# Optimization experiments

Hardware: AMD Instinct MI355X
Metric: run time of the kernel (lower is better)

## Reference

```python
import jax, jax.numpy as jnp
import numpy as np

N = 100000      # nodes
E = 1600000     # edges
F_IN = 128      # num_features
H = 64          # hidden_channels
EPS = 1e-5      # batchnorm eps


def _bn(x, gamma, beta, mean, var):
    # inference-mode BatchNorm1d
    return (x - mean) * jax.lax.rsqrt(var + EPS) * gamma + beta


def setup_inputs() -> dict:
    key = jax.random.key(0)
    ks = jax.random.split(key, 16)

    def lin_w(k, fan_in, fan_out):
        return (jax.random.normal(k, (fan_in, fan_out), jnp.float32)
                * (1.0 / np.sqrt(fan_in)))

    return {
        "x": jax.random.normal(ks[0], (N, F_IN), jnp.float32),
        "edge_index": jax.random.randint(ks[1], (2, E), 0, N, dtype=jnp.int32),
        # node_encoder: Linear(F_IN,H) + BN
        "enc_W": lin_w(ks[2], F_IN, H), "enc_b": jnp.zeros((H,), jnp.float32),
        "enc_g": jnp.ones((H,), jnp.float32), "enc_beta": jnp.zeros((H,), jnp.float32),
        "enc_mean": jnp.zeros((H,), jnp.float32), "enc_var": jnp.ones((H,), jnp.float32),
        # GCNConv layers (PyG: lin without bias, bias added after aggregation)
        "conv1_W": lin_w(ks[3], H, H), "conv1_b": jnp.zeros((H,), jnp.float32),
        "conv2_W": lin_w(ks[4], H, H), "conv2_b": jnp.zeros((H,), jnp.float32),
        # edge_predictor: Linear(2H,H) + BN + Linear(H,1)
        "ep1_W": lin_w(ks[5], 2 * H, H), "ep1_b": jnp.zeros((H,), jnp.float32),
        "ep_g": jnp.ones((H,), jnp.float32), "ep_beta": jnp.zeros((H,), jnp.float32),
        "ep_mean": jnp.zeros((H,), jnp.float32), "ep_var": jnp.ones((H,), jnp.float32),
        "ep2_W": lin_w(ks[6], H, 1), "ep2_b": jnp.zeros((1,), jnp.float32),
    }


def reference(x, edge_index, enc_W, enc_b, enc_g, enc_beta, enc_mean, enc_var,
              conv1_W, conv1_b, conv2_W, conv2_b,
              ep1_W, ep1_b, ep_g, ep_beta, ep_mean, ep_var, ep2_W, ep2_b):
    row, col = edge_index[0], edge_index[1]

    # GCN normalization with added self-loops (symmetric D^-1/2 (A+I) D^-1/2)
    loops = jnp.arange(N, dtype=row.dtype)
    row_sl = jnp.concatenate([row, loops])          # [E+N]
    col_sl = jnp.concatenate([col, loops])
    deg = jax.ops.segment_sum(jnp.ones_like(col_sl, jnp.float32), col_sl, N)
    dinv = jnp.where(deg > 0, jax.lax.rsqrt(jnp.maximum(deg, 1.0)), 0.0)
    norm = dinv[row_sl] * dinv[col_sl]              # [E+N]

    def gcn_conv(h, W, b):
        hw = h @ W                                   # [N,H]
        msg = hw[row_sl] * norm[:, None]             # gather-scale  [E+N,H]
        return jax.ops.segment_sum(msg, col_sl, N) + b  # scatter-add

    # node encoder (inference: dropout = identity)
    h = jax.nn.relu(_bn(x @ enc_W + enc_b, enc_g, enc_beta, enc_mean, enc_var))
    h = jax.nn.relu(gcn_conv(h, conv1_W, conv1_b))
    h = jax.nn.relu(gcn_conv(h, conv2_W, conv2_b))
    node_embeddings = h

    # edge predictor: gather + cat + MLP + sigmoid
    ef = jnp.concatenate([h[row], h[col]], axis=1)   # [E, 2H]
    e = jax.nn.relu(_bn(ef @ ep1_W + ep1_b, ep_g, ep_beta, ep_mean, ep_var))
    edge_pred = jax.nn.sigmoid(e @ ep2_W + ep2_b)    # [E, 1]
    return node_embeddings, edge_pred
```

## Files before the change

### kernel.cpp

```cpp
#include <hip/hip_runtime.h>
#include <hip/hip_bf16.h>
#include <hip/hip_fp16.h>

#define NN 100000
#define NE 1600000
#define FIN 128
#define HD 64
#define NB_MF 1563
#define BSH 8
#define BUCK 256
#define NBUCK 392
#define BCAP 5120
#define CHUNK 4096
#define NCHUNK 391
#define ESPLIT 2
#define NEB (NBUCK*ESPLIT)
#define NFB 6250
#define NAGG 6250

typedef unsigned int uint32;
typedef _Float16 half8 __attribute__((ext_vector_type(8)));
typedef float f32x4 __attribute__((ext_vector_type(4)));
typedef float f32x8 __attribute__((ext_vector_type(8)));

__global__ void __launch_bounds__(256) k_prep(const float* __restrict__ encW, const float* __restrict__ c1W,
                                              const float* __restrict__ c2W, const float* __restrict__ ep1W,
                                              _Float16* __restrict__ wt,
                                              const float* __restrict__ encB, const float* __restrict__ encG,
                                              const float* __restrict__ encBe, const float* __restrict__ encM,
                                              const float* __restrict__ encV,
                                              const float* __restrict__ ep1b, const float* __restrict__ epG,
                                              const float* __restrict__ epBe, const float* __restrict__ epM,
                                              const float* __restrict__ epV,
                                              float* __restrict__ foldEnc, float* __restrict__ foldPre,
                                              int* __restrict__ bcnt, _Float16* __restrict__ bufBzero){
    int blk = blockIdx.x, t = threadIdx.x;
    if(blk < 96){
        int i = blk*256 + t;
        if(i < 8192){
            int n = i >> 7, k = i & 127;
            wt[i] = (_Float16)encW[k*64 + n];
        } else if(i < 12288){
            int j = i - 8192; int n = j >> 6, k = j & 63;
            wt[i] = (_Float16)c1W[k*64 + n];
        } else if(i < 16384){
            int j = i - 12288; int n = j >> 6, k = j & 63;
            wt[i] = (_Float16)c2W[k*64 + n];
        } else {
            int j = i - 16384; int h = j >> 12; int jj = j & 4095;
            int n = jj >> 6, k = jj & 63;
            wt[i] = (_Float16)ep1W[(h*64 + k)*64 + n];
        }
    } else {
        if(t < 64){
            int j = t;
            float s = encG[j]*rsqrtf(encV[j]+1e-5f);
            foldEnc[j]      = s;
            foldEnc[64+j]   = (encB[j]-encM[j])*s + encBe[j];
            float sp = epG[j]*rsqrtf(epV[j]+1e-5f);
            foldPre[j]      = sp;
            foldPre[64+j]   = sp;
            foldPre[128+j]  = sp*(ep1b[j]-epM[j]) + epBe[j];
            foldPre[192+j]  = 0.f;
            bufBzero[j]     = (_Float16)0.f;
        }
        for(int i = t; i < NBUCK; i += 256) bcnt[i] = 0;
    }
}

__global__ void __launch_bounds__(256) k_part(const int* __restrict__ row,
                                              const int* __restrict__ col,
                                              int* __restrict__ bcnt,
                                              uint32* __restrict__ staged,
                                              uint32* __restrict__ posE){
    __shared__ int hist[NBUCK];
    __shared__ int base[NBUCK];
    int t = threadIdx.x;
    int e0 = blockIdx.x * CHUNK;
    int e1 = min(e0 + CHUNK, NE);
    for(int i = t; i < NBUCK; i += 256) hist[i] = 0;
    __syncthreads();
    for(int e = e0 + t; e < e1; e += 256)
        atomicAdd(&hist[col[e] >> BSH], 1);
    __syncthreads();
    for(int i = t; i < NBUCK; i += 256){
        int c = hist[i];
        base[i] = (c > 0) ? atomicAdd(&bcnt[i], c) : 0;
        hist[i] = 0;
    }
    __syncthreads();
    for(int e = e0 + t; e < e1; e += 256){
        int c = col[e], r = row[e];
        int b = c >> BSH;
        int pos = base[b] + atomicAdd(&hist[b], 1);
        if(pos < BCAP){
            staged[(size_t)b*BCAP + pos] = ((uint32)r << BSH) | (uint32)(c & (BUCK-1));
            posE[e] = (uint32)(b*BCAP + pos);
        } else posE[e] = 0xFFFFFFFFu;
    }
}

__global__ void __launch_bounds__(256) k_fill3(const int* __restrict__ bcnt,
                                               const uint32* __restrict__ staged,
                                               int* __restrict__ deg,
                                               int* __restrict__ starts,
                                               float* __restrict__ dinv,
                                               int* __restrict__ csr){
    __shared__ int h[BUCK];
    __shared__ int sc[BUCK];
    __shared__ int red[256];
    __shared__ int lcsr[BCAP];
    int b = blockIdx.x, t = threadIdx.x;
    int part = 0;
    for(int i = t; i < b; i += 256) part += min(bcnt[i], BCAP);
    red[t] = part; __syncthreads();
    for(int off = 128; off > 0; off >>= 1){
        if(t < off) red[t] += red[t+off];
        __syncthreads();
    }
    int base = red[0];
    h[t] = 0;
    __syncthreads();
    int cnt = min(bcnt[b], BCAP);
    const uint32* st = staged + (size_t)b*BCAP;
    for(int i = t; i < cnt; i += 256) atomicAdd(&h[st[i] & (BUCK-1)], 1);
    __syncthreads();
    int v = h[t];
    sc[t] = v; __syncthreads();
    for(int off = 1; off < 256; off <<= 1){
        int a = (t >= off) ? sc[t-off] : 0;
        __syncthreads();
        sc[t] += a;
        __syncthreads();
    }
    int ex = sc[t] - v;
    int n = b*BUCK + t;
    if(n < NN){
        deg[n]    = v;
        starts[n] = base + ex;
        dinv[n]   = rsqrtf((float)(v + 1));
    }
    h[t] = ex;
    __syncthreads();
    for(int i = t; i < cnt; i += 256){
        uint32 u = st[i];
        int p = atomicAdd(&h[u & (BUCK-1)], 1);
        lcsr[p] = (int)(u >> BSH);
    }
    __syncthreads();
    for(int i = t; i < cnt; i += 256) csr[base + i] = lcsr[i];
}

template<int K, bool AF32, bool FOLD, bool RELU, bool SCALE, int OS>
__global__ void __launch_bounds__(256) k_mfma(const void* __restrict__ Ain,
                                              const _Float16* __restrict__ Bt,
                                              const float* __restrict__ fold,
                                              const float* __restrict__ rowscale,
                                              _Float16* __restrict__ outh){
    constexpr int PS = K + 8;
    __shared__ _Float16 As[64*PS];
    __shared__ _Float16 Bs[64*PS];
    int t = threadIdx.x;
    int m0 = blockIdx.x*64;
    int jh = blockIdx.y;
    {
        const _Float16* src = Bt + (size_t)jh*64*K;
        for(int idx = t; idx < 64*(K/8); idx += 256){
            int n = idx/(K/8), c = idx%(K/8);
            *(half8*)&Bs[n*PS + c*8] = *(const half8*)&src[n*K + c*8];
        }
    }
    if(AF32){
        const float* A = (const float*)Ain;
        for(int idx = t; idx < 64*(K/4); idx += 256){
            int r = idx/(K/4), c = idx%(K/4);
            int rowi = m0 + r; if(rowi >= NN) rowi = NN-1;
            float4 v = *(const float4*)&A[(size_t)rowi*K + c*4];
            _Float16* d = &As[r*PS + c*4];
            d[0]=(_Float16)v.x; d[1]=(_Float16)v.y; d[2]=(_Float16)v.z; d[3]=(_Float16)v.w;
        }
    } else {
        const _Float16* A = (const _Float16*)Ain;
        for(int idx = t; idx < 64*(K/8); idx += 256){
            int r = idx/(K/8), c = idx%(K/8);
            int rowi = m0 + r; if(rowi >= NN) rowi = NN-1;
            *(half8*)&As[r*PS + c*8] = *(const half8*)&A[(size_t)rowi*K + c*8];
        }
    }
    __syncthreads();
    int w = t>>6, l = t&63;
    int lm = l&15, q = l>>4;
    f32x4 acc0 = {0.f,0.f,0.f,0.f}, acc1 = {0.f,0.f,0.f,0.f};
    f32x4 acc2 = {0.f,0.f,0.f,0.f}, acc3 = {0.f,0.f,0.f,0.f};
    const _Float16* arow = &As[(w*16+lm)*PS + q*8];
    const _Float16* brow = &Bs[lm*PS + q*8];
    #pragma unroll
    for(int ks = 0; ks < K/32; ks++){
        half8 a  = *(const half8*)(arow + ks*32);
        half8 b0 = *(const half8*)(brow + ks*32);
        half8 b1 = *(const half8*)(brow + 16*PS + ks*32);
        half8 b2 = *(const half8*)(brow + 32*PS + ks*32);
        half8 b3 = *(const half8*)(brow + 48*PS + ks*32);
        acc0 = __builtin_amdgcn_mfma_f32_16x16x32_f16(a, b0, acc0, 0,0,0);
        acc1 = __builtin_amdgcn_mfma_f32_16x16x32_f16(a, b1, acc1, 0,0,0);
        acc2 = __builtin_amdgcn_mfma_f32_16x16x32_f16(a, b2, acc2, 0,0,0);
        acc3 = __builtin_amdgcn_mfma_f32_16x16x32_f16(a, b3, acc3, 0,0,0);
    }
    f32x4 accs[4] = {acc0, acc1, acc2, acc3};
    #pragma unroll
    for(int nt = 0; nt < 4; nt++){
        int col = nt*16 + lm;
        int jcol = jh*64 + col;
        float fs = FOLD ? fold[jcol] : 0.f;
        float fb = FOLD ? fold[OS + jcol] : 0.f;
        #pragma unroll
        for(int r = 0; r < 4; r++){
            int rowi = m0 + w*16 + q*4 + r;
            if(rowi >= NN) continue;
            float v = accs[nt][r];
            if(FOLD) v = v*fs + fb;
            if(RELU) v = fmaxf(v, 0.f);
            if(SCALE) v *= rowscale[rowi];
            outh[(size_t)rowi*OS + jcol] = (_Float16)v;
        }
    }
}

__global__ void __launch_bounds__(256) k_agg4(const _Float16* __restrict__ hb,
                                              const int* __restrict__ starts,
                                              const int* __restrict__ deg,
                                              const int* __restrict__ csr,
                                              const float* __restrict__ dinv,
                                              const float* __restrict__ bias,
                                              _Float16* __restrict__ outh,
                                              float* __restrict__ outf){
    int t = threadIdx.x, w = t>>6, f = t&63;
    int n0 = blockIdx.x*16 + w*4;
    int s0 = __builtin_amdgcn_readfirstlane(starts[n0+0]);
    int s1 = __builtin_amdgcn_readfirstlane(starts[n0+1]);
    int s2 = __builtin_amdgcn_readfirstlane(starts[n0+2]);
    int s3 = __builtin_amdgcn_readfirstlane(starts[n0+3]);
    int d0 = __builtin_amdgcn_readfirstlane(deg[n0+0]);
    int d1 = __builtin_amdgcn_readfirstlane(deg[n0+1]);
    int d2 = __builtin_amdgcn_readfirstlane(deg[n0+2]);
    int d3 = __builtin_amdgcn_readfirstlane(deg[n0+3]);
    float a0 = 0.f, a1 = 0.f, a2 = 0.f, a3 = 0.f;
    int dmax = max(max(d0,d1), max(d2,d3));
    for(int i0 = 0; i0 < dmax; i0 += 64){
        int li0 = (i0+f < d0) ? csr[s0+i0+f] : NN;
        int li1 = (i0+f < d1) ? csr[s1+i0+f] : NN;
        int li2 = (i0+f < d2) ? csr[s2+i0+f] : NN;
        int li3 = (i0+f < d3) ? csr[s3+i0+f] : NN;
        int mm = min(dmax - i0, 64);
        for(int j = 0; j < mm; j += 8){
            float t0 = 0.f, t1 = 0.f, t2 = 0.f, t3 = 0.f;
            #pragma unroll
            for(int u = 0; u < 8; u++){
                int r0 = __builtin_amdgcn_readlane(li0, j+u);
                int r1 = __builtin_amdgcn_readlane(li1, j+u);
                int r2 = __builtin_amdgcn_readlane(li2, j+u);
                int r3 = __builtin_amdgcn_readlane(li3, j+u);
                t0 += (float)hb[(size_t)r0*64 + f];
                t1 += (float)hb[(size_t)r1*64 + f];
                t2 += (float)hb[(size_t)r2*64 + f];
                t3 += (float)hb[(size_t)r3*64 + f];
            }
            a0 += t0; a1 += t1; a2 += t2; a3 += t3;
        }
    }
    float bv = bias[f];
    float dn0 = dinv[n0+0], dn1 = dinv[n0+1], dn2 = dinv[n0+2], dn3 = dinv[n0+3];
    float sf0 = (float)hb[(size_t)(n0+0)*64 + f];
    float sf1 = (float)hb[(size_t)(n0+1)*64 + f];
    float sf2 = (float)hb[(size_t)(n0+2)*64 + f];
    float sf3 = (float)hb[(size_t)(n0+3)*64 + f];
    float o0 = fmaxf((a0 + sf0)*dn0 + bv, 0.f);
    float o1 = fmaxf((a1 + sf1)*dn1 + bv, 0.f);
    float o2 = fmaxf((a2 + sf2)*dn2 + bv, 0.f);
    float o3 = fmaxf((a3 + sf3)*dn3 + bv, 0.f);
    outh[(size_t)(n0+0)*64 + f] = (_Float16)o0;
    outh[(size_t)(n0+1)*64 + f] = (_Float16)o1;
    outh[(size_t)(n0+2)*64 + f] = (_Float16)o2;
    outh[(size_t)(n0+3)*64 + f] = (_Float16)o3;
    if(outf){
        outf[(size_t)(n0+0)*64 + f] = o0;
        outf[(size_t)(n0+1)*64 + f] = o1;
        outf[(size_t)(n0+2)*64 + f] = o2;
        outf[(size_t)(n0+3)*64 + f] = o3;
    }
}

__global__ void __launch_bounds__(512) k_edgeb(const int* __restrict__ bcnt,
                                               const uint32* __restrict__ staged,
                                               const _Float16* __restrict__ pre,
                                               const float* __restrict__ w2,
                                               const float* __restrict__ b2,
                                               _Float16* __restrict__ zqh){
    __shared__ half8 Bl[BUCK*8];
    int t = threadIdx.x;
    int item = ((int)blockIdx.x & 7)*98 + ((int)blockIdx.x >> 3);
    int b = item >> 1, s = item & 1;
    const _Float16* ps = pre;
    for(int idx = t; idx < BUCK*8; idx += 512){
        int rl = idx >> 3, ch = idx & 7;
        int n = (b << BSH) + rl; if(n >= NN) n = NN-1;
        Bl[rl*8 + (ch ^ (rl & 7))] = *(const half8*)(ps + (size_t)n*128 + 64 + ch*8);
    }
    __syncthreads();

    int cnt = min(bcnt[b], BCAP);
    int lo = (cnt * s) >> 1, hi = (cnt * (s+1)) >> 1;
    const uint32* st = staged + (size_t)b*BCAP;
    _Float16* zb = zqh + (size_t)b*BCAP;
    int p  = t & 7;
    int oc = t >> 3;
    f32x8 w2v = *(const f32x8*)(w2 + 8*p);
    float b2v = b2[0];

    auto edot = [&](uint32 u)->float{
        int r  = (int)(u >> BSH);
        int cl = (int)(u & (BUCK-1));
        half8 av = *(const half8*)(ps + (size_t)r*128 + 8*p);
        half8 bv = Bl[cl*8 + (p ^ (cl & 7))];
        half8 sv = av + bv;
        half8 zero8 = {};
        half8 rv = __builtin_elementwise_max(sv, zero8);
        f32x8 fv = __builtin_convertvector(rv, f32x8);
        float z;
        z  = fv[0]*w2v[0] + fv[1]*w2v[1];
        z  = fmaf(fv[2], w2v[2], z); z = fmaf(fv[3], w2v[3], z);
        z  = fmaf(fv[4], w2v[4], z); z = fmaf(fv[5], w2v[5], z);
        z  = fmaf(fv[6], w2v[6], z); z = fmaf(fv[7], w2v[7], z);
        return z;
    };

    int i = lo + oc;
    for(; i + 64 < hi; i += 128){
        uint32 u0 = st[i], u1 = st[i+64];
        float z0 = edot(u0);
        float z1 = edot(u1);
        z0 += __shfl_xor(z0, 1, 64); z1 += __shfl_xor(z1, 1, 64);
        z0 += __shfl_xor(z0, 2, 64); z1 += __shfl_xor(z1, 2, 64);
        z0 += __shfl_xor(z0, 4, 64); z1 += __shfl_xor(z1, 4, 64);
        if(p == 0){
            zb[i]    = (_Float16)(1.f/(1.f+__expf(-(z0+b2v))));
            zb[i+64] = (_Float16)(1.f/(1.f+__expf(-(z1+b2v))));
        }
    }
    for(; i < hi; i += 64){
        uint32 u0 = st[i];
        float z0 = edot(u0);
        z0 += __shfl_xor(z0, 1, 64);
        z0 += __shfl_xor(z0, 2, 64);
        z0 += __shfl_xor(z0, 4, 64);
        if(p == 0) zb[i] = (_Float16)(1.f/(1.f+__expf(-(z0+b2v))));
    }
}

__global__ void __launch_bounds__(256) k_final(const uint32* __restrict__ posE,
                                               const _Float16* __restrict__ zqh,
                                               float* __restrict__ out){
    int e = blockIdx.x*256 + threadIdx.x;
    if(e < NE){
        uint32 pz = posE[e];
        out[e] = (float)zqh[pz < (uint32)(NBUCK*BCAP) ? pz : 0u];
    }
}


extern "C" void kernel_launch(void* const* d_in, const int* in_sizes, int n_in,
                              void* d_out, int out_size, void* d_ws, size_t ws_size,
                              hipStream_t stream){
    const float* x   = (const float*)d_in[0];
    const int* ei    = (const int*)d_in[1];
    const int* row   = ei;
    const int* col   = ei + NE;
    const float* encW = (const float*)d_in[2],  *encB = (const float*)d_in[3];
    const float* encG = (const float*)d_in[4],  *encBe= (const float*)d_in[5];
    const float* encM = (const float*)d_in[6],  *encV = (const float*)d_in[7];
    const float* c1W  = (const float*)d_in[8],  *c1b  = (const float*)d_in[9];
    const float* c2W  = (const float*)d_in[10], *c2b  = (const float*)d_in[11];
    const float* ep1W = (const float*)d_in[12], *ep1b = (const float*)d_in[13];
    const float* epG  = (const float*)d_in[14], *epBe = (const float*)d_in[15];
    const float* epM  = (const float*)d_in[16], *epV  = (const float*)d_in[17];
    const float* ep2W = (const float*)d_in[18], *ep2b = (const float*)d_in[19];

    char* wsc = (char*)d_ws;
    size_t o = 0;
    auto alloc = [&](size_t bytes)->void*{
        void* p = wsc + o; o += (bytes + 255) & ~(size_t)255; return p;
    };
    int*      deg     = (int*)     alloc((size_t)NN*4);
    int*      starts  = (int*)     alloc((size_t)NN*4);
    int*      bcnt    = (int*)     alloc((size_t)NBUCK*4);
    int*      csr     = (int*)     alloc((size_t)NE*4);
    uint32*   staged  = (uint32*)  alloc((size_t)NBUCK*BCAP*4);
    float*    dinv    = (float*)   alloc((size_t)NN*4);
    float*    foldEnc = (float*)   alloc(128*4);
    float*    foldPre = (float*)   alloc(256*4);
    _Float16* wt      = (_Float16*)alloc(24576*2);
    _Float16* bufA    = (_Float16*)alloc((size_t)NN*64*2);
    _Float16* bufB    = (_Float16*)alloc((size_t)(NN+1)*64*2);
    _Float16* preh    = (_Float16*)alloc((size_t)NN*128*2);
    uint32*   posE    = (uint32*)  alloc((size_t)NE*4);
    _Float16* zqh     = (_Float16*)alloc((size_t)NBUCK*BCAP*2);

    float* outp = (float*)d_out;
    float* node_out = outp;
    float* edge_out = outp + (size_t)NN*64;

    k_prep <<<97, 256, 0, stream>>>(encW, c1W, c2W, ep1W, wt,
                                    encB, encG, encBe, encM, encV,
                                    ep1b, epG, epBe, epM, epV,
                                    foldEnc, foldPre, bcnt, bufB + (size_t)NN*64);
    k_part <<<NCHUNK, 256, 0, stream>>>(row, col, bcnt, staged, posE);
    k_fill3<<<NBUCK,  256, 0, stream>>>(bcnt, staged, deg, starts, dinv, csr);

    k_mfma<128,true,true,true,false,64><<<dim3(NB_MF,1), 256, 0, stream>>>
        (x, wt, foldEnc, nullptr, bufA);

    k_mfma<64,false,false,false,true,64><<<dim3(NB_MF,1), 256, 0, stream>>>
        (bufA, wt + 8192, nullptr, dinv, bufB);
    k_agg4 <<<NAGG, 256, 0, stream>>>(bufB, starts, deg, csr, dinv, c1b,
                                      bufA, nullptr);

    k_mfma<64,false,false,false,true,64><<<dim3(NB_MF,1), 256, 0, stream>>>
        (bufA, wt + 12288, nullptr, dinv, bufB);
    k_agg4 <<<NAGG, 256, 0, stream>>>(bufB, starts, deg, csr, dinv, c2b,
                                      bufA, node_out);

    k_mfma<64,false,true,false,false,128><<<dim3(NB_MF,2), 256, 0, stream>>>
        (bufA, wt + 16384, foldPre, nullptr, preh);

    k_edgeb<<<NEB, 512, 0, stream>>>(bcnt, staged, (const _Float16*)preh, ep2W, ep2b, zqh);
    k_final<<<NFB, 256, 0, stream>>>(posE, zqh, edge_out);
}
```

Measured before the change: 334.6 us.

## Sort edge chunk by bucket in LDS before writing staged buckets

The partition kernel now runs a block-wide exclusive scan over bucket counts. It sorts each chunk's edges into shared memory grouped by bucket, then writes them to the global staged array in bucket order. The goal is to turn scattered 4-byte global writes into mostly contiguous runs per bucket and improve write coalescing. In exchange it adds shared-memory use of about 40 KB, two serial scans with many barriers, and an extra LDS pass.

After: 326.6 us. 2.4% less time.

```diff
diff --git a/kernel.cpp b/kernel.cpp
--- a/kernel.cpp
+++ b/kernel.cpp
@@ -73,30 +73,65 @@
                                               int* __restrict__ bcnt,
                                               uint32* __restrict__ staged,
                                               uint32* __restrict__ posE){
-    __shared__ int hist[NBUCK];
-    __shared__ int base[NBUCK];
+    __shared__ int h[512];
+    __shared__ int sc[512];
+    __shared__ int gb[512];
+    __shared__ uint32 lcsr[CHUNK];
+    __shared__ int dst[CHUNK];
     int t = threadIdx.x;
     int e0 = blockIdx.x * CHUNK;
     int e1 = min(e0 + CHUNK, NE);
-    for(int i = t; i < NBUCK; i += 256) hist[i] = 0;
+    h[t] = 0; h[256+t] = 0;
     __syncthreads();
     for(int e = e0 + t; e < e1; e += 256)
-        atomicAdd(&hist[col[e] >> BSH], 1);
-    __syncthreads();
-    for(int i = t; i < NBUCK; i += 256){
-        int c = hist[i];
-        base[i] = (c > 0) ? atomicAdd(&bcnt[i], c) : 0;
-        hist[i] = 0;
+        atomicAdd(&h[col[e] >> BSH], 1);
+    __syncthreads();
+    int c0 = h[t], c1 = h[256+t];
+    int i2 = 256 + t;
+    gb[t]  = (c0 > 0) ? atomicAdd(&bcnt[t], c0) : 0;
+    gb[i2] = (i2 < NBUCK && c1 > 0) ? atomicAdd(&bcnt[i2], c1) : 0;
+    sc[t] = c0; __syncthreads();
+    for(int off = 1; off < 256; off <<= 1){
+        int a = (t >= off) ? sc[t-off] : 0;
+        __syncthreads();
+        sc[t] += a;
+        __syncthreads();
+    }
+    int sum0 = sc[255];
+    __syncthreads();
+    sc[i2] = c1; __syncthreads();
+    for(int off = 1; off < 256; off <<= 1){
+        int a = (t >= off) ? sc[i2-off] : 0;
+        __syncthreads();
+        sc[i2] += a;
+        __syncthreads();
+    }
+    __syncthreads();
+    {
+        int st0 = sc[t] - c0;
+        int st1 = sc[i2] + sum0 - c1;
+        h[t]   = st0;
+        h[i2]  = st1;
+        sc[t]  = t*BCAP  + gb[t]  - st0;
+        sc[i2] = i2*BCAP + gb[i2] - st1;
     }
     __syncthreads();
     for(int e = e0 + t; e < e1; e += 256){
         int c = col[e], r = row[e];
         int b = c >> BSH;
-        int pos = base[b] + atomicAdd(&hist[b], 1);
-        if(pos < BCAP){
-            staged[(size_t)b*BCAP + pos] = ((uint32)r << BSH) | (uint32)(c & (BUCK-1));
-            posE[e] = (uint32)(b*BCAP + pos);
-        } else posE[e] = 0xFFFFFFFFu;
+        int p = atomicAdd(&h[b], 1);
+        lcsr[p] = ((uint32)r << BSH) | (uint32)(c & (BUCK-1));
+        int slot = sc[b] + p;
+        int off  = slot - b*BCAP;
+        bool ok  = (off < BCAP);
+        dst[p]   = ok ? slot : -1;
+        posE[e]  = ok ? (uint32)slot : 0xFFFFFFFFu;
+    }
+    __syncthreads();
+    int cnt = e1 - e0;
+    for(int i = t; i < cnt; i += 256){
+        int d = dst[i];
+        if(d >= 0) staged[d] = lcsr[i];
     }
 }
 
```
